# Performance work log

Measured on AMD Instinct MI355X. Metric: run time of the kernel, lower is better.

The kernel has to match this reference:

```python
import jax, jax.numpy as jnp
import numpy as np

B, S, E, H = 2, 2048, 512, 8
D = E // H
BETA = 0.5
SCALE = float(np.sqrt(D))


def setup_inputs() -> dict:
    key = jax.random.key(0)
    ks = jax.random.split(key, 22)
    inp = {}
    for i, n in enumerate(["qx", "qy", "kx", "ky", "vx", "vy"]):
        inp[n] = jax.random.normal(ks[i], (B, S, E), jnp.float32)
    wnames = ["Wqx", "Wqy", "Wkx", "Wky", "Wvx", "Wvy", "Wox", "Woy"]
    for i, n in enumerate(wnames):
        inp[n] = jax.random.normal(ks[6 + i], (E, E), jnp.float32) * 0.02
        inp["b" + n[1:]] = jnp.zeros((E,), jnp.float32)
    return inp


def _split_heads(x):
    # [B, S, E] -> [B, H, S, D]
    return x.reshape(B, S, H, D).transpose(0, 2, 1, 3)


def _merge_heads(x):
    # [B, H, S, D] -> [B, S, E]
    return x.transpose(0, 2, 1, 3).reshape(B, S, E)


def reference(qx, qy, kx, ky, vx, vy,
              Wqx, bqx, Wqy, bqy, Wkx, bkx, Wky, bky,
              Wvx, bvx, Wvy, bvy, Wox, box, Woy, boy):
    lin = lambda x, W, b: x @ W.T + b  # torch nn.Linear convention
    qxh = _split_heads(lin(qx, Wqx, bqx))
    qyh = _split_heads(lin(qy, Wqy, bqy))
    kxh = _split_heads(lin(kx, Wkx, bkx))
    kyh = _split_heads(lin(ky, Wky, bky))
    vxh = _split_heads(lin(vx, Wvx, bvx))
    vyh = _split_heads(lin(vy, Wvy, bvy))

    # polar decomposition of the bichannel: radius, angle
    aq = jnp.arctan2(qyh, qxh)  # [B,H,S,D]
    ak = jnp.arctan2(kyh, kxh)
    # mean_d cos(aq - ak) == (cos_q @ cos_k^T + sin_q @ sin_k^T) / D
    # (avoids the [B,H,Sq,Sk,D] angle_diff tensor; same math)
    phase = (jnp.einsum('bhqd,bhkd->bhqk', jnp.cos(aq), jnp.cos(ak))
             + jnp.einsum('bhqd,bhkd->bhqk', jnp.sin(aq), jnp.sin(ak))) / D

    rq = jnp.sqrt(qxh * qxh + qyh * qyh)
    rk = jnp.sqrt(kxh * kxh + kyh * kyh)
    mag = jnp.einsum('bhqd,bhkd->bhqk', rq, rk) / SCALE

    scores = BETA * phase + (1.0 - BETA) * mag  # [B,H,Sq,Sk]
    attn = jax.nn.softmax(scores, axis=-1)      # dropout is identity in eval

    ax = _merge_heads(jnp.einsum('bhqk,bhkd->bhqd', attn, vxh))
    ay = _merge_heads(jnp.einsum('bhqk,bhkd->bhqd', attn, vyh))
    return lin(ax, Wox, box), lin(ay, Woy, boy)
```

## Files before the change

### kernel.cpp

```cpp
#include <hip/hip_runtime.h>
#include <hip/hip_bf16.h>


#define N_ROWS 4096
#define EDIM 512
#define SEQ 2048
#define NHEAD 8
#define HDIM 64
#define CDIM 192
#define DV 128

#define PHASE_A 0.08838834764831845f
#define MAG_B   0.25f
#define SM_SHIFT 8.0f

typedef _Float16 half8 __attribute__((ext_vector_type(8)));
typedef float f32x4 __attribute__((ext_vector_type(4)));

__device__ inline void gload16(const void* g, void* l) {
    __builtin_amdgcn_global_load_lds(
        (const __attribute__((address_space(1))) unsigned int*)g,
        (__attribute__((address_space(3))) unsigned int*)l, 16, 0, 0);
}

#define KSW(r) (((((r) & 3) | (((r) >> 1) & 4))) << 4)

struct Cvt8 { const float* s[8]; _Float16* d[8]; };

__global__ __launch_bounds__(256) void cvt_fp16(Cvt8 j, int n8) {
    const float* s = j.s[blockIdx.y];
    _Float16* d = j.d[blockIdx.y];
    union U { _Float16 h[8]; uint4 u; };
    for (int i = blockIdx.x * 256 + threadIdx.x; i < n8; i += gridDim.x * 256) {
        const float4 f0 = ((const float4*)s)[2 * i];
        const float4 f1 = ((const float4*)s)[2 * i + 1];
        U u;
        u.h[0] = (_Float16)f0.x; u.h[1] = (_Float16)f0.y;
        u.h[2] = (_Float16)f0.z; u.h[3] = (_Float16)f0.w;
        u.h[4] = (_Float16)f1.x; u.h[5] = (_Float16)f1.y;
        u.h[6] = (_Float16)f1.z; u.h[7] = (_Float16)f1.w;
        ((uint4*)d)[i] = u.u;
    }
}

struct PairArgs {
    const void* x0;     const void* x1;
    const _Float16* w0; const _Float16* w1;
    const float* b0;    const float* b1;
    void* dst0;         void* dst1;
};

template <int FUSED>
__global__ __launch_bounds__(256, 3) void gemm16(PairArgs A0, PairArgs A1, PairArgs A2)
{
    __shared__ _Float16 smem[2][12288];

    const int tid = threadIdx.x;
    const int w = tid >> 6, l = tid & 63;
    const int g = l >> 4, ql = l & 15;
    const int wr = w >> 1, wc = w & 1;

    const int dd = blockIdx.x;
    const int xcd = dd & 7;
    const int sb = dd >> 3;
    int z_, mt, nb;
    if (FUSED) {
        const int zm = xcd * 12 + (sb >> 3);
        nb = sb & 7;
        z_ = zm >> 5;
        mt = zm & 31;
    } else {
        z_ = 0;
        mt = xcd * 4 + (sb >> 3);
        nb = sb & 7;
    }
    const PairArgs& A = FUSED ? (z_ == 0 ? A0 : (z_ == 1 ? A1 : A2)) : A0;
    const int z = z_;
    const int m0 = mt * 128;
    const int n0 = nb * 64;

    size_t srcA[2];
    #pragma unroll
    for (int i = 0; i < 2; ++i) {
        const int s = i * 256 + tid;
        const int row = s >> 2, c = s & 3;
        const int cs = c ^ ((row >> 1) & 3);
        srcA[i] = (size_t)(m0 + row) * EDIM + cs * 8;
    }
    const int rowB = tid >> 2;
    const int csB = (tid & 3) ^ ((rowB >> 1) & 3);
    const size_t srcB = (size_t)(n0 + rowB) * EDIM + csB * 8;

    const float* x0f = (const float*)A.x0;
    const float* x1f = (const float*)A.x1;
    const _Float16* x0h = (const _Float16*)A.x0;
    const _Float16* x1h = (const _Float16*)A.x1;

    float4 xr[2][2][2];

    #define LOADX(k0)                                                         \
        do { _Pragma("unroll")                                                \
          for (int i = 0; i < 2; ++i) {                                       \
              const float* p0 = x0f + srcA[i] + (k0);                         \
              const float* p1 = x1f + srcA[i] + (k0);                         \
              xr[0][i][0] = *(const float4*)p0;                               \
              xr[0][i][1] = *(const float4*)(p0 + 4);                         \
              xr[1][i][0] = *(const float4*)p1;                               \
              xr[1][i][1] = *(const float4*)(p1 + 4);                         \
          } } while (0)
    #define WRITEX(buf)                                                       \
        do { _Pragma("unroll")                                                \
          for (int arr = 0; arr < 2; ++arr) {                                 \
              _Pragma("unroll")                                               \
              for (int i = 0; i < 2; ++i) {                                   \
                  union { _Float16 h[8]; uint4 u; } t;                        \
                  _Pragma("unroll")                                           \
                  for (int jj = 0; jj < 4; ++jj) {                            \
                      t.h[jj]     = (_Float16)xr[arr][i][0][jj];              \
                      t.h[4 + jj] = (_Float16)xr[arr][i][1][jj];              \
                  }                                                           \
                  *(uint4*)&smem[buf][arr * 4096 + (i * 256 + tid) * 8] = t.u;\
              } } } while (0)
    #define STAGEX_LDS(buf, k0)                                               \
        do { _Pragma("unroll")                                                \
          for (int i = 0; i < 2; ++i) {                                       \
              gload16(x0h + srcA[i] + (k0),                                   \
                      &smem[buf][(i * 256 + w * 64) * 8]);                    \
              gload16(x1h + srcA[i] + (k0),                                   \
                      &smem[buf][4096 + (i * 256 + w * 64) * 8]);             \
          } } while (0)
    #define STAGEW(buf, k0)                                                   \
        do { gload16(A.w0 + srcB + (k0), &smem[buf][8192 + w * 512]);         \
             gload16(A.w1 + srcB + (k0), &smem[buf][10240 + w * 512]); } while (0)

    f32x4 acc0[4][2], acc1[4][2];
    #pragma unroll
    for (int f = 0; f < 4; ++f)
        #pragma unroll
        for (int e = 0; e < 2; ++e) {
            acc0[f][e] = (f32x4){0.f, 0.f, 0.f, 0.f};
            acc1[f][e] = (f32x4){0.f, 0.f, 0.f, 0.f};
        }

    auto COMPUTE = [&](int buf) {
        half8 af0[4], af1[4], bf0[2], bf1[2];
        #pragma unroll
        for (int f = 0; f < 4; ++f) {
            const int arow = wr * 64 + f * 16 + ql;
            const int ho = arow * 32 + (g ^ ((arow >> 1) & 3)) * 8;
            af0[f] = *(const half8*)&smem[buf][ho];
            af1[f] = *(const half8*)&smem[buf][4096 + ho];
        }
        #pragma unroll
        for (int e = 0; e < 2; ++e) {
            const int brow = wc * 32 + e * 16 + ql;
            const int ho = brow * 32 + (g ^ ((brow >> 1) & 3)) * 8;
            bf0[e] = *(const half8*)&smem[buf][8192 + ho];
            bf1[e] = *(const half8*)&smem[buf][10240 + ho];
        }
        #pragma unroll
        for (int f = 0; f < 4; ++f)
            #pragma unroll
            for (int e = 0; e < 2; ++e) {
                acc0[f][e] = __builtin_amdgcn_mfma_f32_16x16x32_f16(
                    af0[f], bf0[e], acc0[f][e], 0, 0, 0);
                acc1[f][e] = __builtin_amdgcn_mfma_f32_16x16x32_f16(
                    af1[f], bf1[e], acc1[f][e], 0, 0, 0);
            }
    };

    if (FUSED) {
        LOADX(0);
        WRITEX(0);
    } else {
        STAGEX_LDS(0, 0);
    }
    STAGEW(0, 0);

    for (int k0 = 0; k0 < EDIM; k0 += 32) {
        const int cur = (k0 >> 5) & 1, nxt = cur ^ 1;
        __syncthreads();
        const bool more = (k0 + 32) < EDIM;
        if (more) {
            if (FUSED) {
                LOADX(k0 + 32);
            } else {
                STAGEX_LDS(nxt, k0 + 32);
            }
            STAGEW(nxt, k0 + 32);
        }
        COMPUTE(cur);
        if (more && FUSED) {
            WRITEX(nxt);
        }
    }
    #undef LOADX
    #undef WRITEX
    #undef STAGEX_LDS
    #undef STAGEW

    #pragma unroll
    for (int f = 0; f < 4; ++f) {
        const int mb = m0 + wr * 64 + f * 16 + g * 4;
        #pragma unroll
        for (int e = 0; e < 2; ++e) {
            const int n = n0 + wc * 32 + e * 16 + ql;
            const float bias0 = A.b0[n];
            const float bias1 = A.b1[n];
            if (!FUSED) {
                float* o0 = (float*)A.dst0;
                float* o1 = (float*)A.dst1;
                #pragma unroll
                for (int r = 0; r < 4; ++r) {
                    const int m = mb + r;
                    o0[(size_t)m * EDIM + n] = acc0[f][e][r] + bias0;
                    o1[(size_t)m * EDIM + n] = acc1[f][e][r] + bias1;
                }
            } else {
                const int b = mb >> 11, s = mb & (SEQ - 1);
                const int h = nb;
                const int d = n & (HDIM - 1);
                const int bh = b * NHEAD + h;
                _Float16* dst = (_Float16*)A.dst0;
                if (z != 2) {
                    const size_t base = ((size_t)bh * SEQ + s) * CDIM + d;
                    #pragma unroll
                    for (int r = 0; r < 4; ++r) {
                        const float v0 = acc0[f][e][r] + bias0;
                        const float v1 = acc1[f][e][r] + bias1;
                        const float r2 = v0 * v0 + v1 * v1;
                        const float rm = sqrtf(r2);
                        float c, sn;
                        if (r2 > 0.f) { c = v0 / rm; sn = v1 / rm; }
                        else          { c = 1.f;     sn = 0.f; }
                        dst[base + (size_t)r * CDIM]       = (_Float16)(c  * PHASE_A);
                        dst[base + (size_t)r * CDIM + 64]  = (_Float16)(sn * PHASE_A);
                        dst[base + (size_t)r * CDIM + 128] = (_Float16)(rm * MAG_B);
                    }
                } else {
                    union Pk { _Float16 h[4]; uint2 u; } p0, p1;
                    #pragma unroll
                    for (int r = 0; r < 4; ++r) {
                        p0.h[r] = (_Float16)(acc0[f][e][r] + bias0);
                        p1.h[r] = (_Float16)(acc1[f][e][r] + bias1);
                    }
                    *(uint2*)&dst[((size_t)bh * DV + d) * SEQ + s]      = p0.u;
                    *(uint2*)&dst[((size_t)bh * DV + 64 + d) * SEQ + s] = p1.u;
                }
            }
        }
    }
}

__global__ __launch_bounds__(512, 2) void attn_mfma(
    const _Float16* __restrict__ Qg, const _Float16* __restrict__ Kg,
    const _Float16* __restrict__ Vg,
    _Float16* __restrict__ ax, _Float16* __restrict__ ay)
{
    __shared__ char smem[81920];

    const int tid = threadIdx.x;
    const int w  = tid >> 6;
    const int l  = tid & 63;
    const int g  = l >> 4;
    const int ql = l & 15;
    const int tg = w >> 1;
    const int kh = w & 1;

    const int d  = blockIdx.x;
    const int xcd = d & 7;
    const int j   = d >> 3;
    const int bh  = xcd + 8 * (j >> 4);
    const int q0  = (j & 15) * 128;
    const int b  = bh >> 3, h = bh & 7;

    half8 qf[2][6];
    #pragma unroll
    for (int hh = 0; hh < 2; ++hh) {
        const int qrow = q0 + tg * 32 + hh * 16 + ql;
        const char* qp = (const char*)(Qg + ((size_t)bh * SEQ + qrow) * CDIM);
        #pragma unroll
        for (int c = 0; c < 6; ++c) {
            uint4 u = *(const uint4*)(qp + c * 64 + g * 16);
            qf[hh][c] = __builtin_bit_cast(half8, u);
        }
    }

    f32x4 o[2][8];
    #pragma unroll
    for (int hh = 0; hh < 2; ++hh)
        #pragma unroll
        for (int vt = 0; vt < 8; ++vt) o[hh][vt] = (f32x4){0.f, 0.f, 0.f, 0.f};
    float l_i[2] = {0.f, 0.f};

    const char* kgb = (const char*)(Kg + (size_t)bh * SEQ * CDIM);
    const char* vgb = (const char*)(Vg + (size_t)bh * DV * SEQ);

    int koff[3], vofs[2];
    #pragma unroll
    for (int i = 0; i < 3; ++i) {
        const int beta = (w * 3 + i) * 1024 + l * 16;
        const int r = beta / 384;
        const int cb = (beta - r * 384) ^ KSW(r);
        koff[i] = r * 384 + cb;
    }
    #pragma unroll
    for (int i = 0; i < 2; ++i) {
        const int beta = (w * 2 + i) * 1024 + l * 16;
        const int r = beta >> 7;
        const int cb = (beta & 127) ^ ((r & 7) << 4);
        vofs[i] = r * 4096 + cb;
    }

    const int rq = ((ql >> 2) << 3) + (ql & 3);
    const int kxor = ((ql & 3) | (((ql >> 2) & 1) << 2)) << 4;

    #define STAGE(kbase, vbase, kt0)                                          \
        do { _Pragma("unroll")                                                \
          for (int i = 0; i < 3; ++i)                                         \
              gload16(kgb + (size_t)(kt0) * 384 + koff[i],                    \
                      smem + (kbase) + (w * 3 + i) * 1024);                   \
          _Pragma("unroll")                                                   \
          for (int i = 0; i < 2; ++i)                                         \
              gload16(vgb + (size_t)(kt0) * 2 + vofs[i],                      \
                      smem + (vbase) + (w * 2 + i) * 1024); } while (0)

    auto COMPUTE = [&](const int kbase, const int vbase) {
        f32x4 st[2][2];
        __builtin_amdgcn_s_setprio(1);
        #pragma unroll
        for (int kt2 = 0; kt2 < 2; ++kt2) {
            f32x4 a0 = {0.f, 0.f, 0.f, 0.f};
            f32x4 a1 = {0.f, 0.f, 0.f, 0.f};
            const int r_p = rq + kh * 32 + (kt2 << 2);
            #pragma unroll
            for (int c = 0; c < 6; ++c) {
                uint4 u = *(const uint4*)(
                    smem + kbase + ((r_p * 384 + c * 64 + g * 16) ^ kxor));
                const half8 kf = __builtin_bit_cast(half8, u);
                a0 = __builtin_amdgcn_mfma_f32_16x16x32_f16(kf, qf[0][c], a0, 0, 0, 0);
                a1 = __builtin_amdgcn_mfma_f32_16x16x32_f16(kf, qf[1][c], a1, 0, 0, 0);
            }
            st[0][kt2] = a0; st[1][kt2] = a1;
        }
        __builtin_amdgcn_s_setprio(0);

        #pragma unroll
        for (int hh = 0; hh < 2; ++hh) {
            float rs = 0.f;
            #pragma unroll
            for (int kt2 = 0; kt2 < 2; ++kt2)
                #pragma unroll
                for (int r = 0; r < 4; ++r) {
                    const float p = __expf(st[hh][kt2][r] - SM_SHIFT);
                    st[hh][kt2][r] = p; rs += p;
                }
            rs += __shfl_xor(rs, 16);
            rs += __shfl_xor(rs, 32);
            l_i[hh] += rs;
        }

        half8 pf[2];
        #pragma unroll
        for (int hh = 0; hh < 2; ++hh) {
            union { _Float16 hhv[8]; half8 v; } u;
            #pragma unroll
            for (int r = 0; r < 4; ++r) {
                u.hhv[r]     = (_Float16)st[hh][0][r];
                u.hhv[4 + r] = (_Float16)st[hh][1][r];
            }
            pf[hh] = u.v;
        }

        __builtin_amdgcn_s_setprio(1);
        #pragma unroll
        for (int vt = 0; vt < 8; ++vt) {
            const int v = vt * 16 + ql;
            uint4 u = *(const uint4*)(
                smem + vbase + ((v * 128 + kh * 64 + g * 16) ^ ((v & 7) << 4)));
            const half8 vf = __builtin_bit_cast(half8, u);
            o[0][vt] = __builtin_amdgcn_mfma_f32_16x16x32_f16(pf[0], vf, o[0][vt], 0, 0, 0);
            o[1][vt] = __builtin_amdgcn_mfma_f32_16x16x32_f16(pf[1], vf, o[1][vt], 0, 0, 0);
        }
        __builtin_amdgcn_s_setprio(0);
    };

    STAGE(0, 49152, 0);
    for (int t = 0; t < 32; t += 2) {
        __syncthreads();
        STAGE(24576, 65536, (t + 1) * 64);
        COMPUTE(0, 49152);
        __syncthreads();
        if (t + 2 < 32) STAGE(0, 49152, (t + 2) * 64);
        COMPUTE(24576, 65536);
    }
    #undef STAGE

    __syncthreads();
    if (kh == 1) {
        char* base = smem + tg * 16384;
        #pragma unroll
        for (int hh = 0; hh < 2; ++hh)
            #pragma unroll
            for (int vt = 0; vt < 8; ++vt)
                *(f32x4*)(base + hh * 8192 + vt * 1024 + l * 16) = o[hh][vt];
        *(float2*)(smem + 65536 + tg * 512 + l * 8) =
            make_float2(l_i[0], l_i[1]);
    }
    __syncthreads();
    if (kh == 0) {
        const char* base = smem + tg * 16384;
        const float2 lp = *(const float2*)(smem + 65536 + tg * 512 + l * 8);
        const float inv0 = 1.f / (l_i[0] + lp.x);
        const float inv1 = 1.f / (l_i[1] + lp.y);
        float fi[2][4];
        #pragma unroll
        for (int r = 0; r < 4; ++r) {
            fi[0][r] = __shfl(inv0, g * 4 + r);
            fi[1][r] = __shfl(inv1, g * 4 + r);
        }
        #pragma unroll
        for (int hh = 0; hh < 2; ++hh) {
            #pragma unroll
            for (int vt = 0; vt < 8; ++vt) {
                const f32x4 op = *(const f32x4*)(base + hh * 8192 + vt * 1024 + l * 16);
                const int v = vt * 16 + ql;
                _Float16* basep = (vt < 4) ? ax : ay;
                const int vv = v & 63;
                #pragma unroll
                for (int r = 0; r < 4; ++r) {
                    const int q = q0 + tg * 32 + hh * 16 + g * 4 + r;
                    basep[((size_t)(b * SEQ + q)) * EDIM + h * HDIM + vv] =
                        (_Float16)((o[hh][vt][r] + op[r]) * fi[hh][r]);
                }
            }
        }
    }
}

extern "C" void kernel_launch(void* const* d_in, const int* in_sizes, int n_in,
                              void* d_out, int out_size, void* d_ws, size_t ws_size,
                              hipStream_t stream)
{
    const float* act[6];
    for (int i = 0; i < 6; ++i) act[i] = (const float*)d_in[i];
    const float* W[8]; const float* Bv[8];
    for (int i = 0; i < 8; ++i) {
        W[i]  = (const float*)d_in[6 + 2 * i];
        Bv[i] = (const float*)d_in[7 + 2 * i];
    }

    float* outx = (float*)d_out;
    float* outy = outx + 2097152;

    _Float16* ws = (_Float16*)d_ws;
    _Float16* w16[8];
    for (int i = 0; i < 8; ++i) w16[i] = ws + (size_t)i * 262144;
    _Float16* Qt16 = ws + 2097152;
    _Float16* Kt16 = Qt16 + 6291456;
    _Float16* Vt16 = Kt16 + 6291456;
    _Float16* ax16 = Vt16 + 4194304;
    _Float16* ay16 = ax16 + 2097152;

    Cvt8 jw{};
    for (int i = 0; i < 8; ++i) { jw.s[i] = W[i]; jw.d[i] = w16[i]; }
    hipLaunchKernelGGL(cvt_fp16, dim3(128, 8), dim3(256), 0, stream, jw, 32768);

    PairArgs qa{act[0], act[1], w16[0], w16[1], Bv[0], Bv[1], Qt16, nullptr};
    PairArgs ka{act[2], act[3], w16[2], w16[3], Bv[2], Bv[3], Kt16, nullptr};
    PairArgs va{act[4], act[5], w16[4], w16[5], Bv[4], Bv[5], Vt16, nullptr};
    hipLaunchKernelGGL((gemm16<1>), dim3(768), dim3(256), 0, stream, qa, ka, va);

    hipLaunchKernelGGL(attn_mfma, dim3(256), dim3(512), 0, stream,
                       Qt16, Kt16, Vt16, ax16, ay16);

    PairArgs oa{ax16, ay16, w16[6], w16[7], Bv[6], Bv[7], outx, outy};
    hipLaunchKernelGGL((gemm16<0>), dim3(256), dim3(256), 0, stream, oa, oa, oa);
}
```

Baseline: 116.8 us.

## Triple-buffer K/V tiles and software-pipeline QK with softmax and PV

Replaces the double-buffered attention loop with a three-stage LDS ring that uses explicit vmcnt waits and raw barriers. The loop is also software-pipelined so the QK MFMAs for the next tile are issued before the exp/PV work on the current tile. The per-tile row-sum shuffles are dropped and the partial sums are reduced once after the loop. The aim is to hide global-load latency and MFMA dependency stalls. In exchange, LDS grows to 120 KB per block, which may cut occupancy below two blocks per CU, and register pressure rises from holding two raw score sets.

```diff
diff --git a/kernel.cpp b/kernel.cpp
--- a/kernel.cpp
+++ b/kernel.cpp
@@ -24,6 +24,9 @@
 }
 
 #define KSW(r) (((((r) & 3) | (((r) >> 1) & 4))) << 4)
+
+#define WAITN(n) do { asm volatile("s_waitcnt vmcnt(" #n ")" ::: "memory"); \
+                      __builtin_amdgcn_sched_barrier(0); } while (0)
 
 struct Cvt8 { const float* s[8]; _Float16* d[8]; };
 
@@ -257,7 +260,7 @@
     const _Float16* __restrict__ Vg,
     _Float16* __restrict__ ax, _Float16* __restrict__ ay)
 {
-    __shared__ char smem[81920];
+    __shared__ char smem[122880];
 
     const int tid = threadIdx.x;
     const int w  = tid >> 6;
@@ -325,9 +328,9 @@
               gload16(vgb + (size_t)(kt0) * 2 + vofs[i],                      \
                       smem + (vbase) + (w * 2 + i) * 1024); } while (0)
 
-    auto COMPUTE = [&](const int kbase, const int vbase) {
-        f32x4 st[2][2];
-        __builtin_amdgcn_s_setprio(1);
+    struct Raw { f32x4 v[2][2]; };
+
+    auto QKRAW = [&](const int kbase, Raw& out) {
         #pragma unroll
         for (int kt2 = 0; kt2 < 2; ++kt2) {
             f32x4 a0 = {0.f, 0.f, 0.f, 0.f};
@@ -341,10 +344,11 @@
                 a0 = __builtin_amdgcn_mfma_f32_16x16x32_f16(kf, qf[0][c], a0, 0, 0, 0);
                 a1 = __builtin_amdgcn_mfma_f32_16x16x32_f16(kf, qf[1][c], a1, 0, 0, 0);
             }
-            st[0][kt2] = a0; st[1][kt2] = a1;
-        }
-        __builtin_amdgcn_s_setprio(0);
-
+            out.v[0][kt2] = a0; out.v[1][kt2] = a1;
+        }
+    };
+
+    auto FINISH = [&](Raw& rw, half8 pf[2]) {
         #pragma unroll
         for (int hh = 0; hh < 2; ++hh) {
             float rs = 0.f;
@@ -352,26 +356,21 @@
             for (int kt2 = 0; kt2 < 2; ++kt2)
                 #pragma unroll
                 for (int r = 0; r < 4; ++r) {
-                    const float p = __expf(st[hh][kt2][r] - SM_SHIFT);
-                    st[hh][kt2][r] = p; rs += p;
+                    const float p = __expf(rw.v[hh][kt2][r] - SM_SHIFT);
+                    rw.v[hh][kt2][r] = p; rs += p;
                 }
-            rs += __shfl_xor(rs, 16);
-            rs += __shfl_xor(rs, 32);
             l_i[hh] += rs;
-        }
-
-        half8 pf[2];
-        #pragma unroll
-        for (int hh = 0; hh < 2; ++hh) {
-            union { _Float16 hhv[8]; half8 v; } u;
+            union { _Float16 hv[8]; half8 v; } u;
             #pragma unroll
             for (int r = 0; r < 4; ++r) {
-                u.hhv[r]     = (_Float16)st[hh][0][r];
-                u.hhv[4 + r] = (_Float16)st[hh][1][r];
+                u.hv[r]     = (_Float16)rw.v[hh][0][r];
+                u.hv[4 + r] = (_Float16)rw.v[hh][1][r];
             }
             pf[hh] = u.v;
         }
-
+    };
+
+    auto PVSTEP = [&](const int vbase, half8 pf[2]) {
         __builtin_amdgcn_s_setprio(1);
         #pragma unroll
         for (int vt = 0; vt < 8; ++vt) {
@@ -385,16 +384,44 @@
         __builtin_amdgcn_s_setprio(0);
     };
 
-    STAGE(0, 49152, 0);
-    for (int t = 0; t < 32; t += 2) {
-        __syncthreads();
-        STAGE(24576, 65536, (t + 1) * 64);
-        COMPUTE(0, 49152);
-        __syncthreads();
-        if (t + 2 < 32) STAGE(0, 49152, (t + 2) * 64);
-        COMPUTE(24576, 65536);
+    int kbA = 0,     kbB = 24576, kbC = 49152;
+    int vbA = 73728, vbB = 90112, vbC = 106496;
+
+    STAGE(kbA, vbA, 0);
+    STAGE(kbB, vbB, 64);
+    STAGE(kbC, vbC, 128);
+    WAITN(10);
+    __builtin_amdgcn_s_barrier();
+
+    Raw rawA, rawB;
+    QKRAW(kbA, rawA);
+
+    for (int t = 0; t < 31; ++t) {
+        if (t == 30) { WAITN(0); } else { WAITN(5); }
+        __builtin_amdgcn_s_barrier();
+        QKRAW(kbB, rawB);
+        half8 pf[2];
+        FINISH(rawA, pf);
+        PVSTEP(vbA, pf);
+        __builtin_amdgcn_s_barrier();
+        if (t + 3 < 32) STAGE(kbA, vbA, (t + 3) * 64);
+        const int tk = kbA, tv = vbA;
+        kbA = kbB; kbB = kbC; kbC = tk;
+        vbA = vbB; vbB = vbC; vbC = tv;
+        rawA = rawB;
+    }
+    {
+        half8 pf[2];
+        FINISH(rawA, pf);
+        PVSTEP(vbA, pf);
     }
     #undef STAGE
+
+    #pragma unroll
+    for (int hh = 0; hh < 2; ++hh) {
+        l_i[hh] += __shfl_xor(l_i[hh], 16);
+        l_i[hh] += __shfl_xor(l_i[hh], 32);
+    }
 
     __syncthreads();
     if (kh == 1) {
```

After: 113.0 us (median of 3 runs). -3.2%, faster.
